# Kernel tuning notes

Hardware: AMD Instinct MI355X
Metric: run time of the kernel (lower is better)

The kernel has to match this reference:

```python
import jax, jax.numpy as jnp
import numpy as np

N, D, E, R, TOPK = 8192, 4096, 8, 128, 2
LORA_ALPHA = 32.0
SCALING = LORA_ALPHA / R


def setup_inputs() -> dict:
    key = jax.random.key(0)
    kx, kr, ka, kb = jax.random.split(key, 4)
    x = jax.random.normal(kx, (N, D), jnp.float32)
    Wr = jax.random.normal(kr, (E, D), jnp.float32) * 0.02  # router Linear weight [E, D]
    br = jnp.zeros((E,), jnp.float32)                        # router bias
    A = jax.random.normal(ka, (E, R, D), jnp.float32) * 0.02  # per-expert lora_A weights
    B = jax.random.normal(kb, (E, D, R), jnp.float32) * 0.02  # per-expert lora_B weights
    return {"x": x, "Wr": Wr, "br": br, "A": A, "B": B}


def reference(x, Wr, br, A, B):
    # Router: softmax over expert logits, top-k, renormalize selected probs.
    logits = x @ Wr.T + br                       # [N, E]
    probs = jax.nn.softmax(logits, axis=-1)
    top_v, top_i = jax.lax.top_k(probs, TOPK)    # [N, K]
    w = top_v / jnp.sum(top_v, axis=-1, keepdims=True)
    # Scatter renormalized weights back to a dense [N, E] gate (0 for unselected).
    n_idx = jnp.arange(x.shape[0])[:, None]
    gate = jnp.zeros_like(probs).at[n_idx, top_i].set(w)
    # Expert LoRA: y_e = (x @ A_e^T) @ B_e^T * scaling; combine with gates.
    h = jnp.einsum('nd,erd->ner', x, A)          # [N, E, R] small rank intermediate
    out = jnp.einsum('ner,ne,eor->no', h, gate, B) * SCALING  # [N, D]
    return out
```

## Files before the change

### kernel.cpp

```cpp
#include <hip/hip_runtime.h>

#define N_TOK 8192
#define DIM   4096
#define NEXP  8
#define RANK  128
#define EK    (NEXP * RANK)
#define SCAL  0.25f

typedef unsigned short u16;
typedef __bf16 bf16x8 __attribute__((ext_vector_type(8)));
typedef float  f32x4  __attribute__((ext_vector_type(4)));

typedef const __attribute__((address_space(1))) void* as1_cvp;
typedef __attribute__((address_space(3))) void*       as3_vp;

__device__ __forceinline__ void async16(void* lds, const void* g) {
  __builtin_amdgcn_global_load_lds((as1_cvp)g, (as3_vp)lds, 16, 0, 0);
}

__device__ __forceinline__ u16 f2bf(float f) {
  unsigned int u = __builtin_bit_cast(unsigned int, f);
  u += 0x7fffu + ((u >> 16) & 1u);
  return (u16)(u >> 16);
}

__device__ __forceinline__ f32x4 mfma16(bf16x8 a, bf16x8 b, f32x4 c) {
  return __builtin_amdgcn_mfma_f32_16x16x32_bf16(a, b, c, 0, 0, 0);
}

#define PIPE_WAIT(N)                                            \
  __builtin_amdgcn_sched_barrier(0);                            \
  asm volatile("s_waitcnt vmcnt(" #N ")" ::: "memory");         \
  __builtin_amdgcn_s_barrier();                                 \
  __builtin_amdgcn_sched_barrier(0)

#define PIPE_END()                                              \
  __builtin_amdgcn_sched_barrier(0);                            \
  __builtin_amdgcn_s_barrier();                                 \
  __builtin_amdgcn_sched_barrier(0)

__global__ __launch_bounds__(256) void cvtA_kernel(const float* __restrict__ A,
                                                   u16* __restrict__ Ab) {
  size_t i = (size_t)blockIdx.x * 256 + threadIdx.x;
  float4 v = ((const float4*)A)[i];
  ushort4 o;
  o.x = f2bf(v.x); o.y = f2bf(v.y); o.z = f2bf(v.z); o.w = f2bf(v.w);
  ((ushort4*)Ab)[i] = o;
}

__global__ __launch_bounds__(256) void cvtB_kernel(const float* __restrict__ B,
                                                   u16* __restrict__ Bt) {
  size_t i = (size_t)blockIdx.x * 256 + threadIdx.x;
  int r4 = (int)(i & 31);
  int o_ = (int)((i >> 5) & 4095);
  int e  = (int)(i >> 17);
  float4 v = ((const float4*)B)[i];
  ushort4 u;
  u.x = f2bf(v.x); u.y = f2bf(v.y); u.z = f2bf(v.z); u.w = f2bf(v.w);
  ((ushort4*)Bt)[(size_t)o_ * 256 + e * 32 + r4] = u;
}

__device__ __forceinline__ void router_finalize(
    int n, const float* l_in, const float* __restrict__ br,
    float* __restrict__ gw, int* __restrict__ sel) {
  float l[NEXP];
#pragma unroll
  for (int e = 0; e < NEXP; ++e) l[e] = l_in[e] + br[e];
  int i0 = 0;
#pragma unroll
  for (int e = 1; e < NEXP; ++e) if (l[e] > l[i0]) i0 = e;
  int i1 = (i0 == 0) ? 1 : 0;
#pragma unroll
  for (int e = 0; e < NEXP; ++e) if (e != i0 && l[e] > l[i1]) i1 = e;
  float w0 = 1.f / (1.f + expf(l[i1] - l[i0]));
  gw[n * 2 + 0] = w0 * SCAL;
  gw[n * 2 + 1] = (1.f - w0) * SCAL;
  sel[n] = i0 | (i1 << 4);
}

__global__ __launch_bounds__(256) void router_kernel(
    const float* __restrict__ x, const float* __restrict__ Wr,
    const float* __restrict__ br, u16* __restrict__ xb,
    float* __restrict__ gw, int* __restrict__ sel) {
  const int tid = threadIdx.x;
  const int wv = tid >> 6, lane = tid & 63;
  const int n0 = (blockIdx.x * 4 + wv) * 2;
  const float4* x4 = (const float4*)x;
  const float4* w4 = (const float4*)Wr;

  const float4* xr0 = x4 + (size_t)n0 * 1024;
  const float4* xr1 = x4 + (size_t)(n0 + 1) * 1024;
  ushort4* xo0 = (ushort4*)(xb + (size_t)n0 * DIM);
  ushort4* xo1 = (ushort4*)(xb + (size_t)(n0 + 1) * DIM);

  float s0[NEXP] = {}, s1[NEXP] = {};
#pragma unroll 4
  for (int it = 0; it < 16; ++it) {
    const int col = it * 64 + lane;
    float4 xv0 = xr0[col];
    float4 xv1 = xr1[col];
    ushort4 o0, o1;
    o0.x = f2bf(xv0.x); o0.y = f2bf(xv0.y); o0.z = f2bf(xv0.z); o0.w = f2bf(xv0.w);
    o1.x = f2bf(xv1.x); o1.y = f2bf(xv1.y); o1.z = f2bf(xv1.z); o1.w = f2bf(xv1.w);
    xo0[col] = o0;
    xo1[col] = o1;
#pragma unroll
    for (int e = 0; e < NEXP; ++e) {
      float4 wv4 = w4[(size_t)e * 1024 + col];
      s0[e] += xv0.x * wv4.x + xv0.y * wv4.y + xv0.z * wv4.z + xv0.w * wv4.w;
      s1[e] += xv1.x * wv4.x + xv1.y * wv4.y + xv1.z * wv4.z + xv1.w * wv4.w;
    }
  }
#pragma unroll
  for (int m = 1; m < 64; m <<= 1)
#pragma unroll
    for (int e = 0; e < NEXP; ++e) {
      s0[e] += __shfl_xor(s0[e], m, 64);
      s1[e] += __shfl_xor(s1[e], m, 64);
    }
  if (lane == 0)      router_finalize(n0,     s0, br, gw, sel);
  else if (lane == 1) router_finalize(n0 + 1, s1, br, gw, sel);
}

__global__ __launch_bounds__(512) void listbuild_kernel(
    const int* __restrict__ sel, int* __restrict__ lists,
    int* __restrict__ cnt) {
  __shared__ int blkCnt[NEXP];
  __shared__ int gBase[NEXP];
  __shared__ int waveOff[8][NEXP];
  const int tid = threadIdx.x;
  const int wv = tid >> 6, lane = tid & 63;
  const int n = blockIdx.x * 512 + tid;
  if (tid < NEXP) blkCnt[tid] = 0;
  __syncthreads();
  const int s = sel[n];
  const int i0 = s & 15, i1 = (s >> 4) & 15;
#pragma unroll
  for (int e = 0; e < NEXP; ++e) {
    unsigned long long m0 = __ballot(i0 == e);
    unsigned long long m1 = __ballot(i1 == e);
    if (lane == 0)
      waveOff[wv][e] = atomicAdd(&blkCnt[e], __popcll(m0) + __popcll(m1));
  }
  __syncthreads();
  if (tid < NEXP) gBase[tid] = atomicAdd(&cnt[tid], blkCnt[tid]);
  __syncthreads();
  const unsigned long long lt = (1ull << lane) - 1;
#pragma unroll
  for (int e = 0; e < NEXP; ++e) {
    unsigned long long m0 = __ballot(i0 == e);
    unsigned long long m1 = __ballot(i1 == e);
    int base = gBase[e] + waveOff[wv][e];
    if (i0 == e) lists[e * N_TOK + base + (int)__popcll(m0 & lt)] = n * 2;
    if (i1 == e)
      lists[e * N_TOK + base + (int)__popcll(m0) + (int)__popcll(m1 & lt)] =
          n * 2 + 1;
  }
}

__global__ __launch_bounds__(256) void gemm1_kernel(
    const u16* __restrict__ xb, const u16* __restrict__ Ab,
    const int* __restrict__ lists, const int* __restrict__ cnt,
    const float* __restrict__ gw, u16* __restrict__ G) {
  const int e = blockIdx.y;
  const int mt = blockIdx.x;
  const int c = cnt[e];
  if (mt * 64 >= c) return;

  __shared__ alignas(16) u16 As[64 * 64];
  __shared__ alignas(16) u16 Bs[128 * 64];
  __shared__ int   tokS[64];
  __shared__ float wS[64];

  const int tid = threadIdx.x;
  if (tid < 64) {
    int idx = mt * 64 + tid;
    int ci = idx < c ? idx : (c - 1);
    int entry = lists[e * N_TOK + ci];
    tokS[tid] = entry >> 1;
    wS[tid] = (idx < c) ? gw[entry] : 0.0f;
  }
  __syncthreads();

  const int lr = tid >> 3;
  const int cg = tid & 7;
  const u16* ga0 = xb + (size_t)tokS[lr] * DIM + cg * 8;
  const u16* ga1 = xb + (size_t)tokS[lr + 32] * DIM + cg * 8;
  const u16* gb  = Ab + (size_t)e * (RANK * DIM) + (size_t)lr * DIM + cg * 8;

  const int lane = tid & 63, wvi = tid >> 6;
  const int wm = wvi >> 1, wn = wvi & 1;
  const int m16 = lane & 15, quad = lane >> 4;

  f32x4 acc[2][4] = {};

  for (int k0 = 0; k0 < DIM; k0 += 64) {
    async16(&As[tid * 8], ga0 + k0);
    async16(&As[tid * 8 + 2048], ga1 + k0);
#pragma unroll
    for (int r = 0; r < 4; ++r)
      async16(&Bs[tid * 8 + r * 2048], gb + (size_t)r * 32 * DIM + k0);
    __syncthreads();
#pragma unroll
    for (int ks = 0; ks < 2; ++ks) {
      const int ko = ks * 32 + quad * 8;
      bf16x8 af[2], bfr[4];
#pragma unroll
      for (int i = 0; i < 2; ++i)
        af[i] = *(const bf16x8*)&As[(wm * 32 + i * 16 + m16) * 64 + ko];
#pragma unroll
      for (int j = 0; j < 4; ++j)
        bfr[j] = *(const bf16x8*)&Bs[(wn * 64 + j * 16 + m16) * 64 + ko];
#pragma unroll
      for (int i = 0; i < 2; ++i)
#pragma unroll
        for (int j = 0; j < 4; ++j) acc[i][j] = mfma16(af[i], bfr[j], acc[i][j]);
    }
    __syncthreads();
  }

#pragma unroll
  for (int i = 0; i < 2; ++i)
#pragma unroll
    for (int rr = 0; rr < 4; ++rr) {
      int row = wm * 32 + i * 16 + quad * 4 + rr;
      if (mt * 64 + row < c) {
        int tk = tokS[row];
        float wgt = wS[row];
        u16* gp = G + (size_t)tk * EK + e * RANK + wn * 64 + m16;
#pragma unroll
        for (int j = 0; j < 4; ++j) gp[j * 16] = f2bf(acc[i][j][rr] * wgt);
      }
    }
}

__global__ __launch_bounds__(512, 2) void gemm2_kernel(
    const u16* __restrict__ G, const u16* __restrict__ Bt,
    float* __restrict__ out) {
  __shared__ alignas(16) u16 ring[4][2][256 * 32];

  const int lin = blockIdx.y * 16 + blockIdx.x;
  const int swz = (lin & 7) * 64 + (lin >> 3);
  const int by = swz >> 4;
  const int bx = swz & 15;

  const int tid = threadIdx.x;
  const int sr = tid >> 2;
  const int sc = (tid & 3) * 8;
  const u16* gA = G  + (size_t)(by * 256 + sr) * EK + sc;
  const u16* gB = Bt + (size_t)(bx * 256 + sr) * EK + sc;

  const int lane = tid & 63, wvi = tid >> 6;
  const int wm = wvi >> 2, wn = wvi & 3;
  const int m16 = lane & 15, quad = lane >> 4;

  f32x4 acc[8][4] = {};

  auto STAGE = [&](int kt, int slot) {
    u16* lA = &ring[slot][0][tid * 8];
    u16* lB = &ring[slot][1][tid * 8];
    const u16* sA = gA + kt * 32;
    const u16* sB = gB + kt * 32;
    async16(lA,        sA);
    async16(lA + 4096, sA + (size_t)128 * EK);
    async16(lB,        sB);
    async16(lB + 4096, sB + (size_t)128 * EK);
  };

  auto COMPUTE = [&](int slot) {
    const u16* As_ = &ring[slot][0][0];
    const u16* Bs_ = &ring[slot][1][0];
    bf16x8 bfr[4];
#pragma unroll
    for (int j = 0; j < 4; ++j)
      bfr[j] = *(const bf16x8*)&Bs_[(wn * 64 + j * 16 + m16) * 32 + quad * 8];
    __builtin_amdgcn_s_setprio(1);
#pragma unroll
    for (int i = 0; i < 8; ++i) {
      bf16x8 af = *(const bf16x8*)&As_[(wm * 128 + i * 16 + m16) * 32 + quad * 8];
#pragma unroll
      for (int j = 0; j < 4; ++j) acc[i][j] = mfma16(af, bfr[j], acc[i][j]);
    }
    __builtin_amdgcn_s_setprio(0);
  };

  STAGE(0, 0);
  STAGE(1, 1);
  STAGE(2, 2);

  for (int t = 0; t < 29; ++t) {
    PIPE_WAIT(8);
    STAGE(t + 3, (t + 3) & 3);
    COMPUTE(t & 3);
    PIPE_END();
  }
  PIPE_WAIT(8); COMPUTE(1); PIPE_END();
  PIPE_WAIT(4); COMPUTE(2); PIPE_END();
  PIPE_WAIT(0); COMPUTE(3); PIPE_END();

#pragma unroll
  for (int i = 0; i < 8; ++i)
#pragma unroll
    for (int rr = 0; rr < 4; ++rr) {
      int row = by * 256 + wm * 128 + i * 16 + quad * 4 + rr;
      float* op = out + (size_t)row * DIM + bx * 256 + wn * 64 + m16;
#pragma unroll
      for (int j = 0; j < 4; ++j) op[j * 16] = acc[i][j][rr];
    }
}

extern "C" void kernel_launch(void* const* d_in, const int* in_sizes, int n_in,
                              void* d_out, int out_size, void* d_ws, size_t ws_size,
                              hipStream_t stream) {
  const float* x  = (const float*)d_in[0];
  const float* Wr = (const float*)d_in[1];
  const float* br = (const float*)d_in[2];
  const float* A  = (const float*)d_in[3];
  const float* B  = (const float*)d_in[4];
  float* out = (float*)d_out;

  char* w = (char*)d_ws;
  u16* xb = (u16*)w;      w += (size_t)N_TOK * DIM * 2;
  u16* G  = (u16*)w;      w += (size_t)N_TOK * EK * 2;
  u16* Ab = (u16*)w;      w += (size_t)NEXP * RANK * DIM * 2;
  u16* Bt = (u16*)w;      w += (size_t)DIM * EK * 2;
  float* gw = (float*)w;  w += (size_t)N_TOK * 2 * 4;
  int* lists = (int*)w;   w += (size_t)NEXP * N_TOK * 4;
  int* sel = (int*)w;     w += (size_t)N_TOK * 4;
  int* cnt = (int*)w;     w += 256;

  hipMemsetAsync(cnt, 0, NEXP * sizeof(int), stream);
  hipMemsetAsync(G, 0, (size_t)N_TOK * EK * 2, stream);

  cvtA_kernel<<<dim3(4096), dim3(256), 0, stream>>>(A, Ab);
  cvtB_kernel<<<dim3(4096), dim3(256), 0, stream>>>(B, Bt);
  router_kernel<<<dim3(1024), dim3(256), 0, stream>>>(x, Wr, br, xb, gw, sel);
  listbuild_kernel<<<dim3(16), dim3(512), 0, stream>>>(sel, lists, cnt);
  gemm1_kernel<<<dim3(128, NEXP), dim3(256), 0, stream>>>(xb, Ab, lists, cnt, gw, G);
  gemm2_kernel<<<dim3(16, 32), dim3(512), 0, stream>>>(G, Bt, out);
}
```

Measured before the change: 475.2 us.

## Pipeline gemm1 K-loop with 4-slot LDS ring and async prefetch

Replaces the single-buffered 64-wide K loop in the expert LoRA-A GEMM with a 4-slot ring of 32-wide K tiles. Three tiles are prefetched ahead with async global-to-LDS loads and partial waits, so memory latency overlaps the MFMA work. It also raises wave priority around the MFMA block. The cost is twice the LDS (48KB versus 24KB), which may reduce occupancy, and the change depends on PIPE_WAIT/PIPE_END macros being defined elsewhere in the file.

After: 446.7 us. -6.0%, faster.

```diff
diff --git a/kernel.cpp b/kernel.cpp
--- a/kernel.cpp
+++ b/kernel.cpp
@@ -167,8 +167,8 @@
   const int c = cnt[e];
   if (mt * 64 >= c) return;
 
-  __shared__ alignas(16) u16 As[64 * 64];
-  __shared__ alignas(16) u16 Bs[128 * 64];
+  __shared__ alignas(16) u16 ringA[4][64 * 32];
+  __shared__ alignas(16) u16 ringB[4][128 * 32];
   __shared__ int   tokS[64];
   __shared__ float wS[64];
 
@@ -182,11 +182,11 @@
   }
   __syncthreads();
 
-  const int lr = tid >> 3;
-  const int cg = tid & 7;
-  const u16* ga0 = xb + (size_t)tokS[lr] * DIM + cg * 8;
-  const u16* ga1 = xb + (size_t)tokS[lr + 32] * DIM + cg * 8;
-  const u16* gb  = Ab + (size_t)e * (RANK * DIM) + (size_t)lr * DIM + cg * 8;
+  const int srow = tid >> 2;
+  const int scol = (tid & 3) * 8;
+  const u16* gA  = xb + (size_t)tokS[srow] * DIM + scol;
+  const u16* gB0 = Ab + (size_t)e * (RANK * DIM) + (size_t)srow * DIM + scol;
+  const u16* gB1 = gB0 + (size_t)64 * DIM;
 
   const int lane = tid & 63, wvi = tid >> 6;
   const int wm = wvi >> 1, wn = wvi & 1;
@@ -194,30 +194,42 @@
 
   f32x4 acc[2][4] = {};
 
-  for (int k0 = 0; k0 < DIM; k0 += 64) {
-    async16(&As[tid * 8], ga0 + k0);
-    async16(&As[tid * 8 + 2048], ga1 + k0);
-#pragma unroll
-    for (int r = 0; r < 4; ++r)
-      async16(&Bs[tid * 8 + r * 2048], gb + (size_t)r * 32 * DIM + k0);
-    __syncthreads();
-#pragma unroll
-    for (int ks = 0; ks < 2; ++ks) {
-      const int ko = ks * 32 + quad * 8;
-      bf16x8 af[2], bfr[4];
-#pragma unroll
-      for (int i = 0; i < 2; ++i)
-        af[i] = *(const bf16x8*)&As[(wm * 32 + i * 16 + m16) * 64 + ko];
-#pragma unroll
-      for (int j = 0; j < 4; ++j)
-        bfr[j] = *(const bf16x8*)&Bs[(wn * 64 + j * 16 + m16) * 64 + ko];
-#pragma unroll
-      for (int i = 0; i < 2; ++i)
-#pragma unroll
-        for (int j = 0; j < 4; ++j) acc[i][j] = mfma16(af[i], bfr[j], acc[i][j]);
-    }
-    __syncthreads();
-  }
+  auto STAGE = [&](int kt, int slot) {
+    const int k0 = kt * 32;
+    async16(&ringA[slot][tid * 8],        gA  + k0);
+    async16(&ringB[slot][tid * 8],        gB0 + k0);
+    async16(&ringB[slot][tid * 8 + 2048], gB1 + k0);
+  };
+
+  auto COMPUTE = [&](int slot) {
+    bf16x8 af[2], bfr[4];
+#pragma unroll
+    for (int j = 0; j < 4; ++j)
+      bfr[j] = *(const bf16x8*)&ringB[slot][(wn * 64 + j * 16 + m16) * 32 + quad * 8];
+#pragma unroll
+    for (int i = 0; i < 2; ++i)
+      af[i] = *(const bf16x8*)&ringA[slot][(wm * 32 + i * 16 + m16) * 32 + quad * 8];
+    __builtin_amdgcn_s_setprio(1);
+#pragma unroll
+    for (int i = 0; i < 2; ++i)
+#pragma unroll
+      for (int j = 0; j < 4; ++j) acc[i][j] = mfma16(af[i], bfr[j], acc[i][j]);
+    __builtin_amdgcn_s_setprio(0);
+  };
+
+  STAGE(0, 0);
+  STAGE(1, 1);
+  STAGE(2, 2);
+
+  for (int t = 0; t < 125; ++t) {
+    PIPE_WAIT(6);
+    STAGE(t + 3, (t + 3) & 3);
+    COMPUTE(t & 3);
+    PIPE_END();
+  }
+  PIPE_WAIT(6); COMPUTE(1); PIPE_END();
+  PIPE_WAIT(3); COMPUTE(2); PIPE_END();
+  PIPE_WAIT(0); COMPUTE(3); PIPE_END();
 
 #pragma unroll
   for (int i = 0; i < 2; ++i)
```
